# Optimization experiments

Hardware: AMD Instinct MI355X
Metric: run time of the kernel (lower is better)

Reference implementation:

```python
import jax, jax.numpy as jnp
import numpy as np

B, L, C = 4, 2048, 1024
H = 16
D = C // H  # head_dim = 64


def _rope(t, cos, sin):
    # t: [B, H, L, D]; cos/sin: [L, D//2] broadcast to [1, 1, L, D//2]
    te = t[..., ::2]
    to = t[..., 1::2]
    c = cos[None, None]
    s = sin[None, None]
    re = te * c - to * s
    ro = te * s + to * c
    # interleave even/odd back: [..., D//2, 2] -> [..., D]
    return jnp.stack([re, ro], axis=-1).reshape(t.shape)


def setup_inputs() -> dict:
    key = jax.random.key(0)
    ks = jax.random.split(key, 5)
    x = jax.random.normal(ks[0], (B, L, C), dtype=jnp.float32)
    # rotary phases: theta_i = 10000^(-2i/D), angles = pos * theta
    inv_freq = 1.0 / (10000.0 ** (np.arange(0, D, 2, dtype=np.float32) / D))
    ang = np.arange(L, dtype=np.float32)[:, None] * inv_freq[None, :]  # [L, D//2]
    cos = jnp.asarray(np.cos(ang))
    sin = jnp.asarray(np.sin(ang))
    w_qkv = jax.random.normal(ks[1], (3 * C, C), dtype=jnp.float32) * (C ** -0.5)
    w_proj = jax.random.normal(ks[2], (C, C), dtype=jnp.float32) * (C ** -0.5)
    b_proj = jnp.zeros((C,), dtype=jnp.float32)
    return {"x": x, "cos": cos, "sin": sin, "w_qkv": w_qkv, "w_proj": w_proj, "b_proj": b_proj}


def reference(x, cos, sin, w_qkv, w_proj, b_proj):
    Bx, Lx, Cx = x.shape
    # QKV projection (torch Linear: y = x @ W.T), then split heads
    qkv = jnp.einsum("blc,fc->blf", x, w_qkv)  # [B, L, 3C]
    qkv = qkv.reshape(Bx, Lx, 3, H, D).transpose(2, 0, 3, 1, 4)  # [3, B, H, L, D]
    q, k, v = qkv[0], qkv[1], qkv[2]
    q = _rope(q, cos, sin)
    k = _rope(k, cos, sin)
    # scaled dot-product attention, non-causal
    scale = D ** -0.5
    scores = jnp.einsum("bhqd,bhkd->bhqk", q, k) * scale
    attn = jax.nn.softmax(scores, axis=-1)
    o = jnp.einsum("bhqk,bhkd->bhqd", attn, v)  # [B, H, L, D]
    o = o.transpose(0, 2, 1, 3).reshape(Bx, Lx, Cx)
    return jnp.einsum("blc,fc->blf", o, w_proj) + b_proj
```

## Files before the change

### kernel.cpp

```cpp
#include <hip/hip_runtime.h>
#include <cstdint>


typedef unsigned short u16;
typedef __attribute__((ext_vector_type(8))) short bf16x8;
typedef __attribute__((ext_vector_type(4))) float f32x4;

#define GLD16(g, l)                                                            \
  __builtin_amdgcn_global_load_lds(                                            \
      (const __attribute__((address_space(1))) void*)(g),                      \
      (__attribute__((address_space(3))) void*)(l), 16, 0, 0)

static __device__ __forceinline__ u16 f32_bf16(float f) {
  union { float f; unsigned u; } v; v.f = f;
  unsigned r = v.u + 0x7FFFu + ((v.u >> 16) & 1u);
  return (u16)(r >> 16);
}
static __device__ __forceinline__ float bf16_f32(u16 h) {
  union { unsigned u; float f; } v; v.u = ((unsigned)h) << 16;
  return v.f;
}
static __device__ __forceinline__ unsigned pack_rne(float a, float b) {
  union { float f; unsigned u; } x, y; x.f = a; y.f = b;
  unsigned ua = x.u + 0x7FFFu + ((x.u >> 16) & 1u);
  unsigned ub = y.u + 0x7FFFu + ((y.u >> 16) & 1u);
  return (ua >> 16) | (ub & 0xFFFF0000u);
}

__global__ void detect_dtype(const unsigned* __restrict__ cosw,
                             unsigned* __restrict__ flag) {
  if (threadIdx.x == 0 && blockIdx.x == 0)
    *flag = (cosw[0] == 0x3F800000u) ? 1u : 0u;
}

__global__ __launch_bounds__(256) void convert_all(
    const void* __restrict__ x, const void* __restrict__ wq,
    const void* __restrict__ wp, const void* __restrict__ cs,
    const void* __restrict__ sn, const void* __restrict__ bs,
    u16* __restrict__ xb, u16* __restrict__ wqb, u16* __restrict__ wpb,
    u16* __restrict__ cb, u16* __restrict__ sb, u16* __restrict__ bb,
    const unsigned* __restrict__ flag) {
  int blk = blockIdx.x;
  const void* src; u16* dst; int i0, n4;
  if (blk < 8192)       { src = x;  dst = xb;  i0 = blk;         n4 = 2097152; }
  else if (blk < 11264) { src = wq; dst = wqb; i0 = blk - 8192;  n4 = 786432; }
  else if (blk < 12288) { src = wp; dst = wpb; i0 = blk - 11264; n4 = 262144; }
  else if (blk < 12352) { src = cs; dst = cb;  i0 = blk - 12288; n4 = 16384; }
  else if (blk < 12416) { src = sn; dst = sb;  i0 = blk - 12352; n4 = 16384; }
  else                  { src = bs; dst = bb;  i0 = blk - 12416; n4 = 256; }
  int i = i0 * 256 + threadIdx.x;
  if (i >= n4) return;
  if (*flag) {
    float4 v = ((const float4*)src)[i];
    uint2 o;
    o.x = pack_rne(v.x, v.y);
    o.y = pack_rne(v.z, v.w);
    ((uint2*)dst)[i] = o;
  } else {
    ((uint2*)dst)[i] = ((const uint2*)src)[i];
  }
}

static __device__ __forceinline__ void gemm_mainloop(
    const u16* __restrict__ A, const u16* __restrict__ Bm, int K,
    int m0, int n0, u16* As, u16* Bs, f32x4 acc[4][4]) {
  const int tid  = threadIdx.x;
  const int lane = tid & 63;
  const int wave = tid >> 6;
  const int n16  = lane & 15;
  const int quad = lane >> 4;
  const int wm = (wave >> 1) * 64;
  const int wn = (wave & 1) * 64;
  const u16* ag = A  + (size_t)(m0 + wave * 16 + (lane >> 2)) * K + (lane & 3) * 8;
  const u16* bg = Bm + (size_t)(n0 + wave * 16 + (lane >> 2)) * K + (lane & 3) * 8;
  u16* al = As + wave * (16 * 32);
  u16* bl = Bs + wave * (16 * 32);
  for (int kt = 0; kt < K; kt += 32) {
    GLD16(ag + kt, al);
    GLD16(ag + (size_t)64 * K + kt, al + 64 * 32);
    GLD16(bg + kt, bl);
    GLD16(bg + (size_t)64 * K + kt, bl + 64 * 32);
    __syncthreads();
    bf16x8 af[4], bf[4];
#pragma unroll
    for (int i = 0; i < 4; i++)
      af[i] = *(const bf16x8*)(As + (wm + i * 16 + n16) * 32 + quad * 8);
#pragma unroll
    for (int j = 0; j < 4; j++)
      bf[j] = *(const bf16x8*)(Bs + (wn + j * 16 + n16) * 32 + quad * 8);
#pragma unroll
    for (int i = 0; i < 4; i++)
#pragma unroll
      for (int j = 0; j < 4; j++)
        acc[i][j] = __builtin_amdgcn_mfma_f32_16x16x32_bf16(af[i], bf[j], acc[i][j], 0, 0, 0);
    __syncthreads();
  }
}

__global__ __launch_bounds__(256) void gemm_qkv(
    const u16* __restrict__ x, const u16* __restrict__ w,
    u16* __restrict__ q_ws, u16* __restrict__ k_ws, u16* __restrict__ vt_ws) {
  __shared__ u16 As[128 * 32];
  __shared__ u16 Bs[128 * 32];
  f32x4 acc[4][4];
#pragma unroll
  for (int i = 0; i < 4; i++)
#pragma unroll
    for (int j = 0; j < 4; j++) acc[i][j] = (f32x4){0.f, 0.f, 0.f, 0.f};
  const int m0 = blockIdx.y * 128;
  const int n0 = blockIdx.x * 128;
  gemm_mainloop(x, w, 1024, m0, n0, As, Bs, acc);
  const int lane = threadIdx.x & 63, wave = threadIdx.x >> 6;
  const int n16 = lane & 15, quad = lane >> 4;
  const int wm = (wave >> 1) * 64, wn = (wave & 1) * 64;
#pragma unroll
  for (int i = 0; i < 4; i++)
#pragma unroll
    for (int j = 0; j < 4; j++) {
      int f = n0 + wn + j * 16 + n16;
      int which = f >> 10;
      int rem = f & 1023;
      int h = rem >> 6, d = rem & 63;
      int l0 = m0 + wm + i * 16 + quad * 4;
      int b = l0 >> 11, l = l0 & 2047;
      if (which == 2) {
        uint2 o;
        o.x = pack_rne(acc[i][j][0], acc[i][j][1]);
        o.y = pack_rne(acc[i][j][2], acc[i][j][3]);
        size_t idx = (((size_t)b * 16 + h) * 64 + d) * 2048 + l;
        *(uint2*)(vt_ws + idx) = o;
      } else {
        u16* dst = (which == 0) ? q_ws : k_ws;
        size_t base = (((size_t)b * 16 + h) * 2048 + l) * 64 + d;
#pragma unroll
        for (int r = 0; r < 4; r++)
          dst[base + (size_t)r * 64] = f32_bf16(acc[i][j][r]);
      }
    }
}

#define NP_ROPE 4194304
__global__ __launch_bounds__(256) void rope_qk(
    u16* __restrict__ q, u16* __restrict__ k,
    const u16* __restrict__ cosp, const u16* __restrict__ sinp) {
  int idx = blockIdx.x * 256 + threadIdx.x;
  u16* t = (idx < NP_ROPE) ? q : k;
  int p = (idx < NP_ROPE) ? idx : idx - NP_ROPE;
  int l = (p >> 5) & 2047;
  int i = p & 31;
  unsigned v = ((unsigned*)t)[p];
  float te = bf16_f32((u16)(v & 0xFFFFu));
  float to = bf16_f32((u16)(v >> 16));
  float c = bf16_f32(cosp[l * 32 + i]);
  float s = bf16_f32(sinp[l * 32 + i]);
  ((unsigned*)t)[p] = pack_rne(te * c - to * s, te * s + to * c);
}

__global__ __launch_bounds__(256) void flash_attn(
    const u16* __restrict__ q_ws, const u16* __restrict__ k_ws,
    const u16* __restrict__ vt_ws, u16* __restrict__ o_ws) {
  __shared__ u16 Ks[64 * 64];
  __shared__ u16 Vs[64 * 64];
  __shared__ u16 Pa[4 * 16 * 72];
  const int bh = blockIdx.y;
  const int q0 = blockIdx.x * 64;
  const int b = bh >> 4, h = bh & 15;
  const int tid = threadIdx.x, lane = tid & 63, wave = tid >> 6;
  const int n16 = lane & 15, quad = lane >> 4;
  const int x7 = n16 & 7;
  const size_t hoff = (size_t)bh * (2048 * 64);

  const u16* qrow = q_ws + hoff + (size_t)(q0 + wave * 16 + n16) * 64;
  const bf16x8 qf0 = *(const bf16x8*)(qrow + quad * 8);
  const bf16x8 qf1 = *(const bf16x8*)(qrow + 32 + quad * 8);

  f32x4 oacc[4];
#pragma unroll
  for (int s = 0; s < 4; s++) oacc[s] = (f32x4){0.f, 0.f, 0.f, 0.f};
  f32x4 lq = (f32x4){0.f, 0.f, 0.f, 0.f};

  const int srow = wave * 8 + (lane >> 3);
  const int sw = (lane & 7) ^ ((lane >> 3) & 7);
  const u16* kg = k_ws + hoff + (size_t)srow * 64 + sw * 8;
  const u16* vg = vt_ws + hoff + (size_t)srow * 2048 + sw * 8;
  u16* kl = Ks + wave * 8 * 64;
  u16* vl = Vs + wave * 8 * 64;
  u16* const pw = Pa + wave * (16 * 72);
  u16* const pst = pw + n16 * 72 + quad * 4;
  const u16* const prd = pw + n16 * 72 + quad * 8;

  for (int kt = 0; kt < 2048; kt += 64) {
    GLD16(kg + (size_t)kt * 64, kl);
    GLD16(kg + (size_t)kt * 64 + 32 * 64, kl + 32 * 64);
    GLD16(vg + kt, vl);
    GLD16(vg + kt + (size_t)32 * 2048, vl + 32 * 64);
    __syncthreads();

    f32x4 sacc[4];
#pragma unroll
    for (int sub = 0; sub < 4; sub++) {
      const u16* krow = Ks + (sub * 16 + n16) * 64;
      bf16x8 kf0 = *(const bf16x8*)(krow + (quad ^ x7) * 8);
      bf16x8 kf1 = *(const bf16x8*)(krow + ((quad + 4) ^ x7) * 8);
      f32x4 z = (f32x4){0.f, 0.f, 0.f, 0.f};
      z = __builtin_amdgcn_mfma_f32_16x16x32_bf16(kf0, qf0, z, 0, 0, 0);
      z = __builtin_amdgcn_mfma_f32_16x16x32_bf16(kf1, qf1, z, 0, 0, 0);
      sacc[sub] = z;
    }

#pragma unroll
    for (int sub = 0; sub < 4; sub++) {
      f32x4 p;
#pragma unroll
      for (int r = 0; r < 4; r++) p[r] = __expf(sacc[sub][r] * 0.125f);
      lq += p;
      uint2 o;
      o.x = pack_rne(p[0], p[1]);
      o.y = pack_rne(p[2], p[3]);
      *(uint2*)(pst + sub * 16) = o;
    }

    bf16x8 pf0 = *(const bf16x8*)(prd);
    bf16x8 pf1 = *(const bf16x8*)(prd + 32);
#pragma unroll
    for (int sd = 0; sd < 4; sd++) {
      const u16* vrow = Vs + (sd * 16 + n16) * 64;
      bf16x8 vf0 = *(const bf16x8*)(vrow + (quad ^ x7) * 8);
      bf16x8 vf1 = *(const bf16x8*)(vrow + ((quad + 4) ^ x7) * 8);
      oacc[sd] = __builtin_amdgcn_mfma_f32_16x16x32_bf16(pf0, vf0, oacc[sd], 0, 0, 0);
      oacc[sd] = __builtin_amdgcn_mfma_f32_16x16x32_bf16(pf1, vf1, oacc[sd], 0, 0, 0);
    }
    __syncthreads();
  }

  float l = lq[0] + lq[1] + lq[2] + lq[3];
  l += __shfl_xor(l, 16, 64);
  l += __shfl_xor(l, 32, 64);
  float linv = 1.0f / l;
#pragma unroll
  for (int r = 0; r < 4; r++) {
    float lr = __shfl(linv, quad * 4 + r, 64);
    int row = q0 + wave * 16 + quad * 4 + r;
    size_t base = ((size_t)b * 2048 + row) * 1024 + h * 64;
#pragma unroll
    for (int sd = 0; sd < 4; sd++)
      o_ws[base + sd * 16 + n16] = f32_bf16(oacc[sd][r] * lr);
  }
}

__global__ __launch_bounds__(256) void gemm_proj(
    const u16* __restrict__ o, const u16* __restrict__ w,
    const u16* __restrict__ bias, float* __restrict__ out) {
  __shared__ u16 As[128 * 32];
  __shared__ u16 Bs[128 * 32];
  f32x4 acc[4][4];
#pragma unroll
  for (int i = 0; i < 4; i++)
#pragma unroll
    for (int j = 0; j < 4; j++) acc[i][j] = (f32x4){0.f, 0.f, 0.f, 0.f};
  const int m0 = blockIdx.y * 128;
  const int n0 = blockIdx.x * 128;
  gemm_mainloop(o, w, 1024, m0, n0, As, Bs, acc);
  const int lane = threadIdx.x & 63, wave = threadIdx.x >> 6;
  const int n16 = lane & 15, quad = lane >> 4;
  const int wm = (wave >> 1) * 64, wn = (wave & 1) * 64;
#pragma unroll
  for (int i = 0; i < 4; i++)
#pragma unroll
    for (int j = 0; j < 4; j++) {
      int f = n0 + wn + j * 16 + n16;
      float bf = bf16_f32(bias[f]);
#pragma unroll
      for (int r = 0; r < 4; r++) {
        int m = m0 + wm + i * 16 + quad * 4 + r;
        out[(size_t)m * 1024 + f] = acc[i][j][r] + bf;
      }
    }
}

extern "C" void kernel_launch(void* const* d_in, const int* in_sizes, int n_in,
                              void* d_out, int out_size, void* d_ws, size_t ws_size,
                              hipStream_t stream) {
  float* out = (float*)d_out;

  u16* ws = (u16*)d_ws;
  u16* xb     = ws;
  u16* wqkvb  = ws + 8388608;
  u16* wprojb = ws + 11534336;
  u16* cosb   = ws + 12582912;
  u16* sinb   = ws + 12648448;
  u16* biasb  = ws + 12713984;
  u16* qb     = ws + 12715008;
  u16* kb     = ws + 21103616;
  u16* vtb    = ws + 29492224;
  u16* ob     = xb;
  unsigned* flag = (unsigned*)((char*)d_ws + 75761664);

  detect_dtype<<<1, 64, 0, stream>>>((const unsigned*)d_in[1], flag);
  convert_all<<<12417, 256, 0, stream>>>(
      d_in[0], d_in[3], d_in[4], d_in[1], d_in[2], d_in[5],
      xb, wqkvb, wprojb, cosb, sinb, biasb, flag);

  gemm_qkv<<<dim3(24, 64), 256, 0, stream>>>(xb, wqkvb, qb, kb, vtb);
  rope_qk<<<32768, 256, 0, stream>>>(qb, kb, cosb, sinb);
  flash_attn<<<dim3(32, 64), 256, 0, stream>>>(qb, kb, vtb, ob);
  gemm_proj<<<dim3(8, 64), 256, 0, stream>>>(ob, wprojb, biasb, out);
}
```

Before: 328.7 us.

## Process two query sub-tiles per wave in flash attention to reuse K/V tiles

Each flash-attention block now covers 128 query rows instead of 64, with every wave handling two 16-row query sub-tiles. Each K/V fragment read from LDS and each global tile load therefore feeds twice the MFMA work, which cuts the load and barrier overhead per unit of compute, at the cost of more registers per thread and half as many blocks. The separate dtype-detect kernel is removed, and each convert block now reads the cos word directly. P is packed to bf16 with the HIP intrinsic instead of the manual rounding code.

```diff
diff --git a/kernel.cpp b/kernel.cpp
--- a/kernel.cpp
+++ b/kernel.cpp
@@ -1,4 +1,5 @@
 #include <hip/hip_runtime.h>
+#include <hip/hip_bf16.h>
 #include <cstdint>
 
 
@@ -26,11 +27,11 @@
   unsigned ub = y.u + 0x7FFFu + ((y.u >> 16) & 1u);
   return (ua >> 16) | (ub & 0xFFFF0000u);
 }
-
-__global__ void detect_dtype(const unsigned* __restrict__ cosw,
-                             unsigned* __restrict__ flag) {
-  if (threadIdx.x == 0 && blockIdx.x == 0)
-    *flag = (cosw[0] == 0x3F800000u) ? 1u : 0u;
+static __device__ __forceinline__ unsigned pack_bf16_hw(float a, float b) {
+  float2 t; t.x = a; t.y = b;
+  __hip_bfloat162 h = __float22bfloat162_rn(t);
+  union { __hip_bfloat162 h; unsigned u; } c; c.h = h;
+  return c.u;
 }
 
 __global__ __launch_bounds__(256) void convert_all(
@@ -38,8 +39,8 @@
     const void* __restrict__ wp, const void* __restrict__ cs,
     const void* __restrict__ sn, const void* __restrict__ bs,
     u16* __restrict__ xb, u16* __restrict__ wqb, u16* __restrict__ wpb,
-    u16* __restrict__ cb, u16* __restrict__ sb, u16* __restrict__ bb,
-    const unsigned* __restrict__ flag) {
+    u16* __restrict__ cb, u16* __restrict__ sb, u16* __restrict__ bb) {
+  const unsigned f32mode = (((const unsigned*)cs)[0] == 0x3F800000u);
   int blk = blockIdx.x;
   const void* src; u16* dst; int i0, n4;
   if (blk < 8192)       { src = x;  dst = xb;  i0 = blk;         n4 = 2097152; }
@@ -50,7 +51,7 @@
   else                  { src = bs; dst = bb;  i0 = blk - 12416; n4 = 256; }
   int i = i0 * 256 + threadIdx.x;
   if (i >= n4) return;
-  if (*flag) {
+  if (f32mode) {
     float4 v = ((const float4*)src)[i];
     uint2 o;
     o.x = pack_rne(v.x, v.y);
@@ -156,28 +157,36 @@
   ((unsigned*)t)[p] = pack_rne(te * c - to * s, te * s + to * c);
 }
 
-__global__ __launch_bounds__(256) void flash_attn(
+__global__ __launch_bounds__(256, 4) void flash_attn(
     const u16* __restrict__ q_ws, const u16* __restrict__ k_ws,
     const u16* __restrict__ vt_ws, u16* __restrict__ o_ws) {
   __shared__ u16 Ks[64 * 64];
   __shared__ u16 Vs[64 * 64];
-  __shared__ u16 Pa[4 * 16 * 72];
+  __shared__ u16 Pa[4 * 32 * 72];
   const int bh = blockIdx.y;
-  const int q0 = blockIdx.x * 64;
+  const int q0 = blockIdx.x * 128;
   const int b = bh >> 4, h = bh & 15;
   const int tid = threadIdx.x, lane = tid & 63, wave = tid >> 6;
   const int n16 = lane & 15, quad = lane >> 4;
   const int x7 = n16 & 7;
   const size_t hoff = (size_t)bh * (2048 * 64);
 
-  const u16* qrow = q_ws + hoff + (size_t)(q0 + wave * 16 + n16) * 64;
-  const bf16x8 qf0 = *(const bf16x8*)(qrow + quad * 8);
-  const bf16x8 qf1 = *(const bf16x8*)(qrow + 32 + quad * 8);
-
-  f32x4 oacc[4];
-#pragma unroll
-  for (int s = 0; s < 4; s++) oacc[s] = (f32x4){0.f, 0.f, 0.f, 0.f};
-  f32x4 lq = (f32x4){0.f, 0.f, 0.f, 0.f};
+  bf16x8 qf[2][2];
+#pragma unroll
+  for (int qb = 0; qb < 2; qb++) {
+    const u16* qrow = q_ws + hoff + (size_t)(q0 + wave * 32 + qb * 16 + n16) * 64;
+    qf[qb][0] = *(const bf16x8*)(qrow + quad * 8);
+    qf[qb][1] = *(const bf16x8*)(qrow + 32 + quad * 8);
+  }
+
+  f32x4 oacc[2][4];
+#pragma unroll
+  for (int qb = 0; qb < 2; qb++)
+#pragma unroll
+    for (int s = 0; s < 4; s++) oacc[qb][s] = (f32x4){0.f, 0.f, 0.f, 0.f};
+  f32x4 lq[2];
+  lq[0] = (f32x4){0.f, 0.f, 0.f, 0.f};
+  lq[1] = (f32x4){0.f, 0.f, 0.f, 0.f};
 
   const int srow = wave * 8 + (lane >> 3);
   const int sw = (lane & 7) ^ ((lane >> 3) & 7);
@@ -185,9 +194,7 @@
   const u16* vg = vt_ws + hoff + (size_t)srow * 2048 + sw * 8;
   u16* kl = Ks + wave * 8 * 64;
   u16* vl = Vs + wave * 8 * 64;
-  u16* const pw = Pa + wave * (16 * 72);
-  u16* const pst = pw + n16 * 72 + quad * 4;
-  const u16* const prd = pw + n16 * 72 + quad * 8;
+  u16* const pw = Pa + wave * (32 * 72);
 
   for (int kt = 0; kt < 2048; kt += 64) {
     GLD16(kg + (size_t)kt * 64, kl);
@@ -196,55 +203,63 @@
     GLD16(vg + kt + (size_t)32 * 2048, vl + 32 * 64);
     __syncthreads();
 
-    f32x4 sacc[4];
 #pragma unroll
     for (int sub = 0; sub < 4; sub++) {
       const u16* krow = Ks + (sub * 16 + n16) * 64;
       bf16x8 kf0 = *(const bf16x8*)(krow + (quad ^ x7) * 8);
       bf16x8 kf1 = *(const bf16x8*)(krow + ((quad + 4) ^ x7) * 8);
-      f32x4 z = (f32x4){0.f, 0.f, 0.f, 0.f};
-      z = __builtin_amdgcn_mfma_f32_16x16x32_bf16(kf0, qf0, z, 0, 0, 0);
-      z = __builtin_amdgcn_mfma_f32_16x16x32_bf16(kf1, qf1, z, 0, 0, 0);
-      sacc[sub] = z;
-    }
-
-#pragma unroll
-    for (int sub = 0; sub < 4; sub++) {
-      f32x4 p;
-#pragma unroll
-      for (int r = 0; r < 4; r++) p[r] = __expf(sacc[sub][r] * 0.125f);
-      lq += p;
-      uint2 o;
-      o.x = pack_rne(p[0], p[1]);
-      o.y = pack_rne(p[2], p[3]);
-      *(uint2*)(pst + sub * 16) = o;
-    }
-
-    bf16x8 pf0 = *(const bf16x8*)(prd);
-    bf16x8 pf1 = *(const bf16x8*)(prd + 32);
+#pragma unroll
+      for (int qb = 0; qb < 2; qb++) {
+        f32x4 z = (f32x4){0.f, 0.f, 0.f, 0.f};
+        z = __builtin_amdgcn_mfma_f32_16x16x32_bf16(kf0, qf[qb][0], z, 0, 0, 0);
+        z = __builtin_amdgcn_mfma_f32_16x16x32_bf16(kf1, qf[qb][1], z, 0, 0, 0);
+        f32x4 p;
+#pragma unroll
+        for (int r = 0; r < 4; r++) p[r] = __expf(z[r] * 0.125f);
+        lq[qb] += p;
+        uint2 o;
+        o.x = pack_bf16_hw(p[0], p[1]);
+        o.y = pack_bf16_hw(p[2], p[3]);
+        *(uint2*)(pw + (qb * 16 + n16) * 72 + quad * 4 + sub * 16) = o;
+      }
+    }
+
+    bf16x8 pf[2][2];
+#pragma unroll
+    for (int qb = 0; qb < 2; qb++) {
+      const u16* prow = pw + (qb * 16 + n16) * 72;
+      pf[qb][0] = *(const bf16x8*)(prow + quad * 8);
+      pf[qb][1] = *(const bf16x8*)(prow + 32 + quad * 8);
+    }
 #pragma unroll
     for (int sd = 0; sd < 4; sd++) {
       const u16* vrow = Vs + (sd * 16 + n16) * 64;
       bf16x8 vf0 = *(const bf16x8*)(vrow + (quad ^ x7) * 8);
       bf16x8 vf1 = *(const bf16x8*)(vrow + ((quad + 4) ^ x7) * 8);
-      oacc[sd] = __builtin_amdgcn_mfma_f32_16x16x32_bf16(pf0, vf0, oacc[sd], 0, 0, 0);
-      oacc[sd] = __builtin_amdgcn_mfma_f32_16x16x32_bf16(pf1, vf1, oacc[sd], 0, 0, 0);
+#pragma unroll
+      for (int qb = 0; qb < 2; qb++) {
+        oacc[qb][sd] = __builtin_amdgcn_mfma_f32_16x16x32_bf16(pf[qb][0], vf0, oacc[qb][sd], 0, 0, 0);
+        oacc[qb][sd] = __builtin_amdgcn_mfma_f32_16x16x32_bf16(pf[qb][1], vf1, oacc[qb][sd], 0, 0, 0);
+      }
     }
     __syncthreads();
   }
 
-  float l = lq[0] + lq[1] + lq[2] + lq[3];
-  l += __shfl_xor(l, 16, 64);
-  l += __shfl_xor(l, 32, 64);
-  float linv = 1.0f / l;
-#pragma unroll
-  for (int r = 0; r < 4; r++) {
-    float lr = __shfl(linv, quad * 4 + r, 64);
-    int row = q0 + wave * 16 + quad * 4 + r;
-    size_t base = ((size_t)b * 2048 + row) * 1024 + h * 64;
-#pragma unroll
-    for (int sd = 0; sd < 4; sd++)
-      o_ws[base + sd * 16 + n16] = f32_bf16(oacc[sd][r] * lr);
+#pragma unroll
+  for (int qb = 0; qb < 2; qb++) {
+    float l = lq[qb][0] + lq[qb][1] + lq[qb][2] + lq[qb][3];
+    l += __shfl_xor(l, 16, 64);
+    l += __shfl_xor(l, 32, 64);
+    float linv = 1.0f / l;
+#pragma unroll
+    for (int r = 0; r < 4; r++) {
+      float lr = __shfl(linv, quad * 4 + r, 64);
+      int row = q0 + wave * 32 + qb * 16 + quad * 4 + r;
+      size_t base = ((size_t)b * 2048 + row) * 1024 + h * 64;
+#pragma unroll
+      for (int sd = 0; sd < 4; sd++)
+        o_ws[base + sd * 16 + n16] = f32_bf16(oacc[qb][sd][r] * lr);
+    }
   }
 }
 
@@ -294,15 +309,13 @@
   u16* kb     = ws + 21103616;
   u16* vtb    = ws + 29492224;
   u16* ob     = xb;
-  unsigned* flag = (unsigned*)((char*)d_ws + 75761664);
-
-  detect_dtype<<<1, 64, 0, stream>>>((const unsigned*)d_in[1], flag);
+
   convert_all<<<12417, 256, 0, stream>>>(
       d_in[0], d_in[3], d_in[4], d_in[1], d_in[2], d_in[5],
-      xb, wqkvb, wprojb, cosb, sinb, biasb, flag);
+      xb, wqkvb, wprojb, cosb, sinb, biasb);
 
   gemm_qkv<<<dim3(24, 64), 256, 0, stream>>>(xb, wqkvb, qb, kb, vtb);
   rope_qk<<<32768, 256, 0, stream>>>(qb, kb, cosb, sinb);
-  flash_attn<<<dim3(32, 64), 256, 0, stream>>>(qb, kb, vtb, ob);
+  flash_attn<<<dim3(16, 64), 256, 0, stream>>>(qb, kb, vtb, ob);
   gemm_proj<<<dim3(8, 64), 256, 0, stream>>>(ob, wprojb, biasb, out);
 }
```

After: 320.3 us. 1.03x faster.
